# Optimization experiments

Hardware: AMD Instinct MI355X
Metric: run time of the kernel (lower is better)

The kernel has to match this reference:

```python
import jax, jax.numpy as jnp
import numpy as np

N, K, CI, CO = 1024, 16, 32, 32


def _elu(x):
    return jnp.where(x > 0, x, jnp.expm1(x))


def _eq22(adj, W, b):
    # adj: [B, D, m, m]; W: [15, D, S]; 15 permutation-equivariant basis ops (Maron et al.)
    B, D, m, _ = adj.shape
    mf = jnp.asarray(m, adj.dtype)
    eye = jnp.eye(m, dtype=adj.dtype)
    diag = jnp.diagonal(adj, axis1=2, axis2=3)          # [B,D,m]
    sr = adj.sum(3) / mf                                 # row sums
    sc = adj.sum(2) / mf                                 # col sums
    sd = diag.sum(-1) / mf                               # [B,D]
    sa = adj.sum((2, 3)) / (mf * mf)                     # [B,D]
    full = adj.shape
    bc = lambda t: jnp.broadcast_to(t, full)
    d2m = lambda v: v[..., :, None] * eye
    s2d = lambda s: s[..., None, None] * eye
    s2a = lambda s: jnp.broadcast_to(s[..., None, None], full)
    ops = jnp.stack([
        d2m(diag), s2d(sd), d2m(sr), d2m(sc), s2d(sa),
        bc(sc[..., None, :]), bc(sr[..., None, :]),
        bc(sc[..., :, None]), bc(sr[..., :, None]),
        adj, jnp.swapaxes(adj, 2, 3),
        bc(diag[..., None, :]), bc(diag[..., :, None]),
        s2a(sd), s2a(sa),
    ])  # [15,B,D,m,m]
    return jnp.einsum('pds,pbdij->bsij', W, ops) + b[None, :, None, None]


def _eq21(adj, W, b):
    # adj: [B,D,m,m] -> [B,S,m]; 5 basis ops
    m = adj.shape[-1]
    mf = jnp.asarray(m, adj.dtype)
    diag = jnp.diagonal(adj, axis1=2, axis2=3)
    sr = adj.sum(3) / mf
    sc = adj.sum(2) / mf
    sd = diag.sum(-1) / mf
    sa = adj.sum((2, 3)) / (mf * mf)
    vshape = diag.shape
    ops = jnp.stack([
        diag, sr, sc,
        jnp.broadcast_to(sd[..., None], vshape),
        jnp.broadcast_to(sa[..., None], vshape),
    ])
    return jnp.einsum('pds,pbdi->bsi', W, ops) + b[None, :, None]


def _eq12(x, W, b):
    # x: [B,D,m] -> [B,S,m,m]; 5 basis ops
    B, D, m = x.shape
    mf = jnp.asarray(m, x.dtype)
    eye = jnp.eye(m, dtype=x.dtype)
    s = x.sum(-1) / mf
    full = (B, D, m, m)
    ops = jnp.stack([
        x[..., :, None] * eye,
        s[..., None, None] * eye,
        jnp.broadcast_to(x[..., None, :], full),
        jnp.broadcast_to(x[..., :, None], full),
        jnp.broadcast_to(s[..., None, None], full),
    ])
    return jnp.einsum('pds,pbdij->bsij', W, ops) + b[None, :, None, None]


def _eq11(x, W, b):
    # x: [B,D,m] -> [B,S,m]; 2 basis ops
    mf = jnp.asarray(x.shape[-1], x.dtype)
    s = x.sum(-1) / mf
    ops = jnp.stack([x, jnp.broadcast_to(s[..., None], x.shape)])
    return jnp.einsum('pds,pbdi->bsi', W, ops) + b[None, :, None]


def _forward(x1, A, w22, b22, w21, b21, w12, b12, w11, b11, nbrs):
    n = x1.shape[0]
    # subgraph extraction: gather per-node neighbor features and dense sub-adjacency
    x_sub = jnp.transpose(x1[nbrs], (0, 2, 1))                                      # [N,Ci,K]
    adj_sub = jnp.transpose(A[nbrs[:, :, None], nbrs[:, None, :]], (0, 3, 1, 2))    # [N,Ci,K,K]
    adj_o = jnp.concatenate([_eq22(adj_sub, w22, b22), _eq12(x_sub, w12, b12)], axis=1)  # [N,2S,K,K]
    x_o = jnp.concatenate([_eq21(adj_sub, w21, b21), _eq11(x_sub, w11, b11)], axis=1)    # [N,2S,K]
    c2 = adj_o.shape[1]
    # scatter-mean subgraph edges back to global edge id = src*n + dst
    eid = (nbrs[:, :, None] * n + nbrs[:, None, :]).reshape(-1)
    ev = jnp.transpose(adj_o, (0, 2, 3, 1)).reshape(-1, c2)
    esum = jax.ops.segment_sum(ev, eid, num_segments=n * n)
    ecnt = jax.ops.segment_sum(jnp.ones(eid.shape, ev.dtype), eid, num_segments=n * n)
    edge_attr = _elu(esum / jnp.maximum(ecnt, 1.0)[:, None])
    # scatter-mean subgraph nodes back to global nodes
    nid = nbrs.reshape(-1)
    nv = jnp.transpose(x_o, (0, 2, 1)).reshape(-1, c2)
    nsum = jax.ops.segment_sum(nv, nid, num_segments=n)
    ncnt = jax.ops.segment_sum(jnp.ones(nid.shape, nv.dtype), nid, num_segments=n)
    x_nodes = _elu(nsum / jnp.maximum(ncnt, 1.0)[:, None])
    return edge_attr, x_nodes


def setup_inputs() -> dict:
    key = jax.random.key(0)
    ks = jax.random.split(key, 12)
    return {
        'x1': jax.random.normal(ks[0], (N, CI), jnp.float32),
        'A': jax.random.normal(ks[1], (N, N, CI), jnp.float32),
        'w22': jax.random.normal(ks[2], (15, CI, CO), jnp.float32) * 0.1,
        'b22': jax.random.normal(ks[3], (CO,), jnp.float32) * 0.1,
        'w21': jax.random.normal(ks[4], (5, CI, CO), jnp.float32) * 0.1,
        'b21': jax.random.normal(ks[5], (CO,), jnp.float32) * 0.1,
        'w12': jax.random.normal(ks[6], (5, CI, CO), jnp.float32) * 0.1,
        'b12': jax.random.normal(ks[7], (CO,), jnp.float32) * 0.1,
        'w11': jax.random.normal(ks[8], (2, CI, CO), jnp.float32) * 0.1,
        'b11': jax.random.normal(ks[9], (CO,), jnp.float32) * 0.1,
        'nbrs': jax.random.randint(ks[10], (N, K), 0, N),
    }


def reference(x1, A, w22, b22, w21, b21, w12, b12, w11, b11, nbrs):
    return _forward(x1, A, w22, b22, w21, b21, w12, b12, w11, b11, nbrs)
```

## Files before the change

### kernel.cpp

```cpp
#include <hip/hip_runtime.h>
#include <hip/hip_bf16.h>

#define NN 1024
#define KK 16
#define CI_ 32
#define CO_ 32
#define CAP 64
#define ECAP 8
#define DCAP 128

__device__ __forceinline__ float elu_f(float x) {
    return x > 0.0f ? x : expm1f(x);
}

#define ECNT_OFF   0
#define DCNT_OFF   (1024*1024)
#define INVCNT_OFF (DCNT_OFF + 1024)
#define INVBUF_OFF (INVCNT_OFF + 1024)
#define EBUF_OFF   (INVBUF_OFF + 1024*CAP)
#define DBUF_OFF   (EBUF_OFF + 1024*1024*ECAP)
#define XSTG_OFF   (DBUF_OFF + 1024*DCAP)
#define ASTG_OFF   (XSTG_OFF + 1024*1024)

__global__ __launch_bounds__(256, 2) void subgraph_kernel(
    const float* __restrict__ x1, const float* __restrict__ A,
    const float* __restrict__ w22, const float* __restrict__ b22,
    const float* __restrict__ w21, const float* __restrict__ b21,
    const float* __restrict__ w12, const float* __restrict__ b12,
    const float* __restrict__ w11, const float* __restrict__ b11,
    const int* __restrict__ nbrs,
    float* __restrict__ adj_stage, float* __restrict__ x_stage,
    unsigned int* __restrict__ ecnt, unsigned int* __restrict__ dcnt,
    unsigned int* __restrict__ invcnt, unsigned int* __restrict__ invbuf,
    unsigned int* __restrict__ ebuf, unsigned int* __restrict__ dbuf)
{
    const int b = blockIdx.x;
    const int t = threadIdx.x;

    __shared__ float adjS[32][257];
    __shared__ float xS[32][17];
    __shared__ float w10L[32][32];
    __shared__ float w11L[32][32];
    __shared__ float diagL[32][17], srL[32][17], scL[32][17];
    __shared__ float sdL[32], saL[32], sxL[32];
    __shared__ float rowp[32][17], colp[32][17], diagp[32][17];
    __shared__ float constp[32], dconst22[32];
    __shared__ float xi12[32][17], xj12[32][17], d12t[32][17];
    __shared__ float c12[32], dconst12[32];
    __shared__ float o21[32][17], o11[32][17];
    __shared__ int u[16];

    if (t < 16) u[t] = nbrs[b * KK + t];
    __syncthreads();

    if (t < 16) {
        unsigned int pos = atomicAdd(invcnt + u[t], 1u);
        if (pos < CAP) invbuf[(unsigned)u[t] * CAP + pos] = ((unsigned)b << 4) | (unsigned)t;
    }
    {
        const int pi = t >> 4, pj = t & 15;
        const unsigned vv = (unsigned)u[pi], ww = (unsigned)u[pj];
        const unsigned src = (unsigned)b * 256u + (unsigned)t;
        if (vv == ww) {
            unsigned pos = atomicAdd(dcnt + vv, 1u);
            if (pos < DCAP) dbuf[vv * DCAP + pos] = src;
        } else {
            const unsigned eid = vv * NN + ww;
            unsigned pos = atomicAdd(ecnt + eid, 1u);
            if (pos < ECAP) ebuf[(size_t)eid * ECAP + pos] = src;
        }
    }

    {
        const int pi = t >> 4, pj = t & 15;
        const float4* arow = reinterpret_cast<const float4*>(
            A + ((size_t)u[pi] * NN + (size_t)u[pj]) * CI_);
        #pragma unroll
        for (int q = 0; q < 8; ++q) {
            float4 r = arow[q];
            adjS[4*q+0][t] = r.x; adjS[4*q+1][t] = r.y;
            adjS[4*q+2][t] = r.z; adjS[4*q+3][t] = r.w;
        }
    }
    if (t < 128) {
        const int xi = t >> 3, q = t & 7;
        float4 v = reinterpret_cast<const float4*>(x1 + (size_t)u[xi] * CI_)[q];
        xS[4*q+0][xi] = v.x; xS[4*q+1][xi] = v.y;
        xS[4*q+2][xi] = v.z; xS[4*q+3][xi] = v.w;
    }
    for (int k = t; k < 1024; k += 256) {
        const int d = k >> 5, s = k & 31;
        w10L[d][s] = w22[9  * 1024 + k];
        w11L[d][s] = w22[10 * 1024 + k];
    }
    __syncthreads();

    {
        const int d = t & 31;
        for (int ii = t >> 5; ii < 16; ii += 8) {
            float s_r = 0.f, s_c = 0.f;
            #pragma unroll
            for (int jj = 0; jj < 16; ++jj) {
                s_r += adjS[d][ii * 16 + jj];
                s_c += adjS[d][jj * 16 + ii];
            }
            srL[d][ii] = s_r * (1.f / 16.f);
            scL[d][ii] = s_c * (1.f / 16.f);
            diagL[d][ii] = adjS[d][ii * 16 + ii];
        }
    }
    __syncthreads();
    if (t < 32) {
        float a = 0.f, dd = 0.f, xx = 0.f;
        #pragma unroll
        for (int ii = 0; ii < 16; ++ii) {
            a += srL[t][ii]; dd += diagL[t][ii]; xx += xS[t][ii];
        }
        saL[t] = a * (1.f / 16.f);
        sdL[t] = dd * (1.f / 16.f);
        sxL[t] = xx * (1.f / 16.f);
    }
    __syncthreads();

    {
        const int s = t & 31;
        for (int ii = t >> 5; ii < 16; ii += 8) {
            {
                float rp = 0.f, cp = 0.f, dp = 0.f, o21v = 0.f;
                #pragma unroll 4
                for (int d = 0; d < 32; ++d) {
                    const int wi = d * 32 + s;
                    const float di = diagL[d][ii], sr_ = srL[d][ii], sc_ = scL[d][ii];
                    rp   += w22[7*1024 + wi]*sc_ + w22[8*1024 + wi]*sr_ + w22[12*1024 + wi]*di;
                    cp   += w22[5*1024 + wi]*sc_ + w22[6*1024 + wi]*sr_ + w22[11*1024 + wi]*di;
                    dp   += w22[0*1024 + wi]*di  + w22[2*1024 + wi]*sr_ + w22[3*1024  + wi]*sc_;
                    o21v += w21[0*1024 + wi]*di  + w21[1*1024 + wi]*sr_ + w21[2*1024  + wi]*sc_
                          + w21[3*1024 + wi]*sdL[d] + w21[4*1024 + wi]*saL[d];
                }
                rowp[s][ii] = rp; colp[s][ii] = cp; diagp[s][ii] = dp;
                o21[s][ii]  = o21v + b21[s];
            }
            {
                float xiv = 0.f, xjv = 0.f, d12v = 0.f, o11v = 0.f;
                #pragma unroll 4
                for (int d = 0; d < 32; ++d) {
                    const int wi = d * 32 + s;
                    const float xv = xS[d][ii];
                    xjv  += w12[2*1024 + wi]*xv;
                    xiv  += w12[3*1024 + wi]*xv;
                    d12v += w12[0*1024 + wi]*xv;
                    o11v += w11[0*1024 + wi]*xv + w11[1*1024 + wi]*sxL[d];
                }
                xj12[s][ii] = xjv; xi12[s][ii] = xiv; d12t[s][ii] = d12v;
                o11[s][ii]  = o11v + b11[s];
            }
        }
        if (t < 32) {
            float cpv = 0.f, dc22 = 0.f, c12v = 0.f, dc12 = 0.f;
            #pragma unroll 4
            for (int d = 0; d < 32; ++d) {
                const int wi = d * 32 + t;
                cpv  += w22[13*1024 + wi]*sdL[d] + w22[14*1024 + wi]*saL[d];
                dc22 += w22[1*1024  + wi]*sdL[d] + w22[4*1024  + wi]*saL[d];
                c12v += w12[4*1024  + wi]*sxL[d];
                dc12 += w12[1*1024  + wi]*sxL[d];
            }
            constp[t]   = cpv + b22[t];
            dconst22[t] = dc22;
            c12[t]      = c12v + b12[t];
            dconst12[t] = dc12;
        }
    }
    __syncthreads();

    {
        const int pi = t >> 4, pj = t & 15;
        const bool isdiag = (pi == pj);
        const int pt = pj * 16 + pi;
        float4* e4 = reinterpret_cast<float4*>(adj_stage + ((size_t)b * 256 + t) * 64);

        #pragma unroll
        for (int h = 0; h < 2; ++h) {
            float acc[16];
            #pragma unroll
            for (int s16 = 0; s16 < 16; ++s16) {
                const int s = h * 16 + s16;
                float v = rowp[s][pi] + colp[s][pj] + constp[s];
                if (isdiag) v += diagp[s][pi] + dconst22[s];
                acc[s16] = v;
            }
            #pragma unroll 8
            for (int d = 0; d < 32; ++d) {
                const float a  = adjS[d][t];
                const float at = adjS[d][pt];
                #pragma unroll
                for (int s16 = 0; s16 < 16; ++s16)
                    acc[s16] = fmaf(a, w10L[d][h*16+s16], fmaf(at, w11L[d][h*16+s16], acc[s16]));
            }
            #pragma unroll
            for (int q = 0; q < 4; ++q)
                e4[h*4 + q] = make_float4(acc[4*q], acc[4*q+1], acc[4*q+2], acc[4*q+3]);
        }

        #pragma unroll
        for (int q = 0; q < 8; ++q) {
            float vv[4];
            #pragma unroll
            for (int r = 0; r < 4; ++r) {
                const int s = 4*q + r;
                float v = xj12[s][pj] + xi12[s][pi] + c12[s];
                if (isdiag) v += d12t[s][pi] + dconst12[s];
                vv[r] = v;
            }
            e4[8 + q] = make_float4(vv[0], vv[1], vv[2], vv[3]);
        }
    }

    for (int k = t; k < 1024; k += 256) {
        const int ii = k >> 6, c = k & 63;
        const float v = (c < 32) ? o21[c][ii] : o11[c - 32][ii];
        x_stage[((size_t)b * 16 + ii) * 64 + c] = v;
    }
}

__global__ __launch_bounds__(256) void gather_kernel(
    const float* __restrict__ adj_stage, const float* __restrict__ x_stage,
    const unsigned int* __restrict__ ecnt, const unsigned int* __restrict__ dcnt,
    const unsigned int* __restrict__ invcnt, const unsigned int* __restrict__ invbuf,
    const unsigned int* __restrict__ ebuf, const unsigned int* __restrict__ dbuf,
    float* __restrict__ out)
{
    const int bid = blockIdx.x;
    const int grp = threadIdx.x >> 4;
    const int ln  = threadIdx.x & 15;

    if (bid < 65536) {
        const unsigned eid = (unsigned)bid * 16u + (unsigned)grp;
        const unsigned v = eid >> 10, w = eid & 1023u;
        unsigned cnt;
        const unsigned* list;
        if (v == w) {
            cnt = dcnt[v]; if (cnt > DCAP) cnt = DCAP;
            list = dbuf + v * DCAP;
        } else {
            cnt = ecnt[eid]; if (cnt > ECAP) cnt = ECAP;
            list = ebuf + (size_t)eid * ECAP;
        }
        float4 acc = make_float4(0.f, 0.f, 0.f, 0.f);
        for (unsigned p = 0; p < cnt; ++p) {
            const unsigned src = list[p];
            float4 f = reinterpret_cast<const float4*>(adj_stage + (size_t)src * 64)[ln];
            acc.x += f.x; acc.y += f.y; acc.z += f.z; acc.w += f.w;
        }
        const unsigned full = (v == w) ? dcnt[v] : ecnt[eid];
        const float inv = full ? 1.0f / (float)full : 0.0f;
        acc.x = elu_f(acc.x * inv); acc.y = elu_f(acc.y * inv);
        acc.z = elu_f(acc.z * inv); acc.w = elu_f(acc.w * inv);
        reinterpret_cast<float4*>(out + (size_t)eid * 64)[ln] = acc;
    } else {
        const unsigned v = (unsigned)(bid - 65536) * 16u + (unsigned)grp;
        unsigned cnt = invcnt[v]; if (cnt > CAP) cnt = CAP;
        float4 acc = make_float4(0.f, 0.f, 0.f, 0.f);
        for (unsigned p = 0; p < cnt; ++p) {
            const unsigned e = invbuf[v * CAP + p];
            float4 f = reinterpret_cast<const float4*>(x_stage + (size_t)e * 64)[ln];
            acc.x += f.x; acc.y += f.y; acc.z += f.z; acc.w += f.w;
        }
        const unsigned full = invcnt[v];
        const float inv = full ? 1.0f / (float)full : 0.0f;
        acc.x = elu_f(acc.x * inv); acc.y = elu_f(acc.y * inv);
        acc.z = elu_f(acc.z * inv); acc.w = elu_f(acc.w * inv);
        reinterpret_cast<float4*>(out + (size_t)NN * NN * 64 + (size_t)v * 64)[ln] = acc;
    }
}

extern "C" void kernel_launch(void* const* d_in, const int* in_sizes, int n_in,
                              void* d_out, int out_size, void* d_ws, size_t ws_size,
                              hipStream_t stream) {
    (void)in_sizes; (void)n_in; (void)out_size; (void)ws_size;
    const float* x1   = (const float*)d_in[0];
    const float* A    = (const float*)d_in[1];
    const float* w22  = (const float*)d_in[2];
    const float* b22  = (const float*)d_in[3];
    const float* w21  = (const float*)d_in[4];
    const float* b21  = (const float*)d_in[5];
    const float* w12  = (const float*)d_in[6];
    const float* b12  = (const float*)d_in[7];
    const float* w11  = (const float*)d_in[8];
    const float* b11  = (const float*)d_in[9];
    const int*   nbrs = (const int*)d_in[10];

    float* out = (float*)d_out;
    unsigned int* ws_u = (unsigned int*)d_ws;
    unsigned int* ecnt   = ws_u + ECNT_OFF;
    unsigned int* dcnt   = ws_u + DCNT_OFF;
    unsigned int* invcnt = ws_u + INVCNT_OFF;
    unsigned int* invbuf = ws_u + INVBUF_OFF;
    unsigned int* ebuf   = ws_u + EBUF_OFF;
    unsigned int* dbuf   = ws_u + DBUF_OFF;
    float* x_stage   = (float*)(ws_u + XSTG_OFF);
    float* adj_stage = (float*)(ws_u + ASTG_OFF);

    hipMemsetAsync(ecnt, 0, (size_t)(1024 * 1024 + 2048) * sizeof(unsigned int), stream);

    subgraph_kernel<<<NN, 256, 0, stream>>>(
        x1, A, w22, b22, w21, b21, w12, b12, w11, b11, nbrs,
        adj_stage, x_stage, ecnt, dcnt, invcnt, invbuf, ebuf, dbuf);

    gather_kernel<<<65536 + 64, 256, 0, stream>>>(
        adj_stage, x_stage, ecnt, dcnt, invcnt, invbuf, ebuf, dbuf, out);
}
```

Measured before the change: 583.6 us.

## Gather only touched edges via compacted worklist; zero-fill untouched outputs

Subgraph kernel appends each newly touched off-diagonal edge id to a compacted worklist when its counter goes 0->1. The finalize kernel zero-fills untouched edges with one thread per float4 instead of a 16-lane group doing count checks, and runs gather work only over worklist entries plus the diagonal and node ranges. This avoids scanning the count and list for every one of the 1M edges. In exchange it adds one global atomic per new edge and launches many extra blocks (sized to the worklist cap) that exit early.

```diff
diff --git a/kernel.cpp b/kernel.cpp
--- a/kernel.cpp
+++ b/kernel.cpp
@@ -8,6 +8,7 @@
 #define CAP 64
 #define ECAP 8
 #define DCAP 128
+#define WLCAP 262144
 
 __device__ __forceinline__ float elu_f(float x) {
     return x > 0.0f ? x : expm1f(x);
@@ -16,8 +17,10 @@
 #define ECNT_OFF   0
 #define DCNT_OFF   (1024*1024)
 #define INVCNT_OFF (DCNT_OFF + 1024)
-#define INVBUF_OFF (INVCNT_OFF + 1024)
-#define EBUF_OFF   (INVBUF_OFF + 1024*CAP)
+#define WLCNT_OFF  (INVCNT_OFF + 1024)
+#define INVBUF_OFF (WLCNT_OFF + 1024)
+#define WL_OFF     (INVBUF_OFF + 1024*CAP)
+#define EBUF_OFF   (WL_OFF + WLCAP)
 #define DBUF_OFF   (EBUF_OFF + 1024*1024*ECAP)
 #define XSTG_OFF   (DBUF_OFF + 1024*DCAP)
 #define ASTG_OFF   (XSTG_OFF + 1024*1024)
@@ -32,7 +35,8 @@
     float* __restrict__ adj_stage, float* __restrict__ x_stage,
     unsigned int* __restrict__ ecnt, unsigned int* __restrict__ dcnt,
     unsigned int* __restrict__ invcnt, unsigned int* __restrict__ invbuf,
-    unsigned int* __restrict__ ebuf, unsigned int* __restrict__ dbuf)
+    unsigned int* __restrict__ ebuf, unsigned int* __restrict__ dbuf,
+    unsigned int* __restrict__ wlcnt, unsigned int* __restrict__ wl)
 {
     const int b = blockIdx.x;
     const int t = threadIdx.x;
@@ -68,6 +72,10 @@
             const unsigned eid = vv * NN + ww;
             unsigned pos = atomicAdd(ecnt + eid, 1u);
             if (pos < ECAP) ebuf[(size_t)eid * ECAP + pos] = src;
+            if (pos == 0u) {
+                unsigned slot = atomicAdd(wlcnt, 1u);
+                if (slot < WLCAP) wl[slot] = eid;
+            }
         }
     }
 
@@ -223,50 +231,74 @@
     }
 }
 
-__global__ __launch_bounds__(256) void gather_kernel(
+__global__ __launch_bounds__(256) void finalize_kernel(
     const float* __restrict__ adj_stage, const float* __restrict__ x_stage,
     const unsigned int* __restrict__ ecnt, const unsigned int* __restrict__ dcnt,
     const unsigned int* __restrict__ invcnt, const unsigned int* __restrict__ invbuf,
     const unsigned int* __restrict__ ebuf, const unsigned int* __restrict__ dbuf,
+    const unsigned int* __restrict__ wlcnt, const unsigned int* __restrict__ wl,
     float* __restrict__ out)
 {
     const int bid = blockIdx.x;
+    if (bid < 65536) {
+        const unsigned gid = (unsigned)bid * 256u + (unsigned)threadIdx.x;
+        const unsigned eid = gid >> 4, ln = gid & 15u;
+        const unsigned v = eid >> 10, w = eid & 1023u;
+        const unsigned cnt = (v == w) ? dcnt[v] : ecnt[eid];
+        if (cnt == 0u)
+            reinterpret_cast<float4*>(out + (size_t)eid * 64)[ln] =
+                make_float4(0.f, 0.f, 0.f, 0.f);
+        return;
+    }
+
     const int grp = threadIdx.x >> 4;
     const int ln  = threadIdx.x & 15;
-
-    if (bid < 65536) {
-        const unsigned eid = (unsigned)bid * 16u + (unsigned)grp;
-        const unsigned v = eid >> 10, w = eid & 1023u;
-        unsigned cnt;
-        const unsigned* list;
-        if (v == w) {
-            cnt = dcnt[v]; if (cnt > DCAP) cnt = DCAP;
-            list = dbuf + v * DCAP;
-        } else {
-            cnt = ecnt[eid]; if (cnt > ECAP) cnt = ECAP;
-            list = ebuf + (size_t)eid * ECAP;
-        }
+    const unsigned gidx = (unsigned)(bid - 65536) * 16u + (unsigned)grp;
+
+    if (gidx < WLCAP) {
+        unsigned nwl = *wlcnt; if (nwl > WLCAP) nwl = WLCAP;
+        if (gidx >= nwl) return;
+        const unsigned eid = wl[gidx];
+        const unsigned full = ecnt[eid];
+        unsigned cnt = full; if (cnt > ECAP) cnt = ECAP;
+        const unsigned* list = ebuf + (size_t)eid * ECAP;
         float4 acc = make_float4(0.f, 0.f, 0.f, 0.f);
         for (unsigned p = 0; p < cnt; ++p) {
             const unsigned src = list[p];
             float4 f = reinterpret_cast<const float4*>(adj_stage + (size_t)src * 64)[ln];
             acc.x += f.x; acc.y += f.y; acc.z += f.z; acc.w += f.w;
         }
-        const unsigned full = (v == w) ? dcnt[v] : ecnt[eid];
-        const float inv = full ? 1.0f / (float)full : 0.0f;
+        const float inv = 1.0f / (float)full;
         acc.x = elu_f(acc.x * inv); acc.y = elu_f(acc.y * inv);
         acc.z = elu_f(acc.z * inv); acc.w = elu_f(acc.w * inv);
         reinterpret_cast<float4*>(out + (size_t)eid * 64)[ln] = acc;
-    } else {
-        const unsigned v = (unsigned)(bid - 65536) * 16u + (unsigned)grp;
-        unsigned cnt = invcnt[v]; if (cnt > CAP) cnt = CAP;
+    } else if (gidx < WLCAP + 1024u) {
+        const unsigned v = gidx - WLCAP;
+        const unsigned full = dcnt[v];
+        if (full == 0u) return;
+        unsigned cnt = full; if (cnt > DCAP) cnt = DCAP;
+        const unsigned* list = dbuf + v * DCAP;
+        float4 acc = make_float4(0.f, 0.f, 0.f, 0.f);
+        for (unsigned p = 0; p < cnt; ++p) {
+            const unsigned src = list[p];
+            float4 f = reinterpret_cast<const float4*>(adj_stage + (size_t)src * 64)[ln];
+            acc.x += f.x; acc.y += f.y; acc.z += f.z; acc.w += f.w;
+        }
+        const float inv = 1.0f / (float)full;
+        acc.x = elu_f(acc.x * inv); acc.y = elu_f(acc.y * inv);
+        acc.z = elu_f(acc.z * inv); acc.w = elu_f(acc.w * inv);
+        const unsigned eid = (v << 10) | v;
+        reinterpret_cast<float4*>(out + (size_t)eid * 64)[ln] = acc;
+    } else if (gidx < WLCAP + 2048u) {
+        const unsigned v = gidx - WLCAP - 1024u;
+        const unsigned full = invcnt[v];
+        unsigned cnt = full; if (cnt > CAP) cnt = CAP;
         float4 acc = make_float4(0.f, 0.f, 0.f, 0.f);
         for (unsigned p = 0; p < cnt; ++p) {
             const unsigned e = invbuf[v * CAP + p];
             float4 f = reinterpret_cast<const float4*>(x_stage + (size_t)e * 64)[ln];
             acc.x += f.x; acc.y += f.y; acc.z += f.z; acc.w += f.w;
         }
-        const unsigned full = invcnt[v];
         const float inv = full ? 1.0f / (float)full : 0.0f;
         acc.x = elu_f(acc.x * inv); acc.y = elu_f(acc.y * inv);
         acc.z = elu_f(acc.z * inv); acc.w = elu_f(acc.w * inv);
@@ -295,18 +327,21 @@
     unsigned int* ecnt   = ws_u + ECNT_OFF;
     unsigned int* dcnt   = ws_u + DCNT_OFF;
     unsigned int* invcnt = ws_u + INVCNT_OFF;
+    unsigned int* wlcnt  = ws_u + WLCNT_OFF;
     unsigned int* invbuf = ws_u + INVBUF_OFF;
+    unsigned int* wl     = ws_u + WL_OFF;
     unsigned int* ebuf   = ws_u + EBUF_OFF;
     unsigned int* dbuf   = ws_u + DBUF_OFF;
     float* x_stage   = (float*)(ws_u + XSTG_OFF);
     float* adj_stage = (float*)(ws_u + ASTG_OFF);
 
-    hipMemsetAsync(ecnt, 0, (size_t)(1024 * 1024 + 2048) * sizeof(unsigned int), stream);
+    hipMemsetAsync(ecnt, 0, (size_t)(1024 * 1024 + 3072) * sizeof(unsigned int), stream);
 
     subgraph_kernel<<<NN, 256, 0, stream>>>(
         x1, A, w22, b22, w21, b21, w12, b12, w11, b11, nbrs,
-        adj_stage, x_stage, ecnt, dcnt, invcnt, invbuf, ebuf, dbuf);
-
-    gather_kernel<<<65536 + 64, 256, 0, stream>>>(
-        adj_stage, x_stage, ecnt, dcnt, invcnt, invbuf, ebuf, dbuf, out);
+        adj_stage, x_stage, ecnt, dcnt, invcnt, invbuf, ebuf, dbuf, wlcnt, wl);
+
+    const int gblocks = 65536 + (WLCAP + 2048) / 16;
+    finalize_kernel<<<gblocks, 256, 0, stream>>>(
+        adj_stage, x_stage, ecnt, dcnt, invcnt, invbuf, ebuf, dbuf, wlcnt, wl, out);
 }
```

New measurement: 557.4 us. 1.05x faster.
